# Kernel optimization log

Measured on AMD Instinct MI355X. Metric: run time of the kernel, lower is better.

## Reference

```python
import jax, jax.numpy as jnp
import numpy as np
import math

LS1 = [0, 1, 2]
LS2 = [0, 1, 2]
B = 1048576


def _fact(n):
    return math.factorial(n)


def _w3j_complex(j1, j2, j3, m1, m2, m3):
    # Racah formula for the complex-basis Wigner 3j symbol.
    if m1 + m2 + m3 != 0:
        return 0.0
    if not (abs(j1 - j2) <= j3 <= j1 + j2):
        return 0.0
    if abs(m1) > j1 or abs(m2) > j2 or abs(m3) > j3:
        return 0.0
    tmin = max(0, j2 - j3 - m1, j1 - j3 + m2)
    tmax = min(j1 + j2 - j3, j1 - m1, j2 + m2)
    s = 0.0
    for t in range(tmin, tmax + 1):
        s += (-1) ** t / (
            _fact(t) * _fact(j3 - j2 + t + m1) * _fact(j3 - j1 + t - m2)
            * _fact(j1 + j2 - j3 - t) * _fact(j1 - t - m1) * _fact(j2 - t + m2)
        )
    delta = math.sqrt(
        _fact(j1 + j2 - j3) * _fact(j1 - j2 + j3) * _fact(-j1 + j2 + j3)
        / _fact(j1 + j2 + j3 + 1)
    )
    pref = math.sqrt(
        _fact(j1 + m1) * _fact(j1 - m1) * _fact(j2 + m2) * _fact(j2 - m2)
        * _fact(j3 + m3) * _fact(j3 - m3)
    )
    return ((-1) ** (j1 - j2 - m3)) * delta * pref * s


def _U(l):
    # Unitary change of basis: complex spherical harmonics -> real spherical harmonics.
    d = 2 * l + 1
    U = np.zeros((d, d), dtype=complex)
    s = 1.0 / math.sqrt(2.0)
    for m in range(-l, l + 1):
        i = m + l
        if m > 0:
            U[i, m + l] = ((-1) ** m) * s
            U[i, -m + l] = s
        elif m == 0:
            U[i, l] = 1.0
        else:
            a = -m
            U[i, m + l] = 1j * s
            U[i, a + l] = -1j * ((-1) ** a) * s
    return U


def _real_w3j(l1, l2, l3):
    # Wigner 3j tensor in the real spherical-harmonic basis, Frobenius norm 1.
    W = np.zeros((2 * l1 + 1, 2 * l2 + 1, 2 * l3 + 1), dtype=complex)
    for m1 in range(-l1, l1 + 1):
        for m2 in range(-l2, l2 + 1):
            for m3 in range(-l3, l3 + 1):
                W[m1 + l1, m2 + l2, m3 + l3] = _w3j_complex(l1, l2, l3, m1, m2, m3)
    T = np.einsum('am,bn,co,mno->abc', _U(l1), _U(l2), _U(l3), W)
    re, im = T.real, T.imag
    T = re if np.abs(re).sum() >= np.abs(im).sum() else im
    return T.astype(np.float32)


def build_cb_matrix(ls1, ls2):
    # Faithful replication of EinsumTensorProduct.__init__ layout logic.
    layout = {}
    cb_height = 0
    idx1 = 0
    for l1 in ls1:
        idx2 = 0
        for l2 in ls2:
            for l3 in range(abs(l1 - l2), l1 + l2 + 1):
                layout.setdefault(l3, []).append((l1, l2, idx1, idx2))
                cb_height += 2 * l3 + 1
            idx2 += 2 * l2 + 1
        idx1 += 2 * l1 + 1
    dim1 = sum(2 * l + 1 for l in ls1)
    dim2 = sum(2 * l + 1 for l in ls2)
    cb = np.zeros((cb_height, dim1, dim2), dtype=np.float32)
    lmax2 = max(ls2)
    row = 0
    for l3 in sorted(layout.keys()):
        mults = sorted(layout[l3], key=lambda x: x[0] * lmax2 + x[1])
        for l1, l2, o1, o2 in mults:
            blk = _real_w3j(l1, l2, l3) * math.sqrt(2 * l3 + 1)  # [m1, m2, m3]
            cb[row:row + 2 * l3 + 1, o1:o1 + 2 * l1 + 1, o2:o2 + 2 * l2 + 1] = \
                np.transpose(blk, (2, 0, 1))
            row += 2 * l3 + 1
    return cb


def setup_inputs() -> dict:
    key = jax.random.key(0)
    k1, k2 = jax.random.split(key)
    dim1 = sum(2 * l + 1 for l in LS1)
    dim2 = sum(2 * l + 1 for l in LS2)
    cb = jnp.asarray(build_cb_matrix(LS1, LS2))  # [81, 9, 9]
    in1 = jax.random.normal(k1, (B, dim1), dtype=jnp.float32)
    in2 = jax.random.normal(k2, (B, dim2), dtype=jnp.float32)
    return {"in1": in1, "in2": in2, "cb_matrix": cb}


def reference(in1, in2, cb_matrix):
    # out[b, k] = sum_{i,j} in1[b, i] * in2[b, j] * cb[k, i, j]
    return jnp.einsum('bi,bj,kij->bk', in1, in2, cb_matrix)
```

## Files before the change

### kernel.cpp

```cpp
#include <hip/hip_runtime.h>
#include <stdint.h>

#define THREADS 192
#define ROWS_PER_ITER 192
#define DIM 9
#define NK 81
#define F 81
#define NCHUNK 6
#define NGROUP 12

typedef __attribute__((ext_vector_type(8))) short short8;
typedef __attribute__((ext_vector_type(16))) float f32x16;

__device__ inline unsigned short f32_bf16(float x) {
    unsigned u = __float_as_uint(x);
    u += 0x7FFFu + ((u >> 16) & 1u);
    return (unsigned short)(u >> 16);
}
__device__ inline float bf16_f32(unsigned short h) {
    return __uint_as_float(((unsigned)h) << 16);
}

__global__ __launch_bounds__(THREADS, 3)
void tp_mfma(const float* __restrict__ in1, const float* __restrict__ in2,
             const float* __restrict__ cb, float* __restrict__ out,
             int nrows, int niter) {
    __shared__ __attribute__((aligned(16))) unsigned short s_p[NGROUP * ROWS_PER_ITER * 8];

    const int tid  = threadIdx.x;
    const int lane = tid & 63;
    const int wave = tid >> 6;
    const int l31  = lane & 31;
    const int h    = lane >> 5;
    const int kcol = 32 * wave + l31;

    short8 Bhi[NCHUNK], Blo[NCHUNK];
    for (int c = 0; c < NCHUNK; ++c) {
        union { short8 v; unsigned short u[8]; } bh, bl;
        for (int j = 0; j < 8; ++j) {
            int f = c * 16 + h * 8 + j;
            float v = 0.0f;
            if (f < F && kcol < NK) v = cb[kcol * F + f];
            unsigned short hi = f32_bf16(v);
            bh.u[j] = (unsigned short)hi;
            bl.u[j] = f32_bf16(v - bf16_f32(hi));
        }
        Bhi[c] = bh.v; Blo[c] = bl.v;
    }

    for (int iter = blockIdx.x; iter < niter; iter += gridDim.x) {
        const long rowbase = (long)iter * ROWS_PER_ITER;
        const long row = rowbase + tid;

        __syncthreads();

        float a[DIM], b[DIM];
        if (row < nrows) {
            const float* p1 = in1 + row * DIM;
            const float* p2 = in2 + row * DIM;
#pragma unroll
            for (int i = 0; i < DIM; ++i) { a[i] = p1[i]; b[i] = p2[i]; }
        } else {
#pragma unroll
            for (int i = 0; i < DIM; ++i) { a[i] = 0.0f; b[i] = 0.0f; }
        }
#pragma unroll
        for (int g = 0; g < NGROUP; ++g) {
            unsigned int d[4];
#pragma unroll
            for (int q = 0; q < 4; ++q) {
                const int f0 = g * 8 + 2 * q, f1 = f0 + 1;
                unsigned short h0 = (f0 < F) ? f32_bf16(a[f0 / DIM] * b[f0 % DIM]) : (unsigned short)0;
                unsigned short h1 = (f1 < F) ? f32_bf16(a[f1 / DIM] * b[f1 % DIM]) : (unsigned short)0;
                d[q] = (unsigned)h0 | ((unsigned)h1 << 16);
            }
            ((uint4*)s_p)[g * ROWS_PER_ITER + tid] = make_uint4(d[0], d[1], d[2], d[3]);
        }
        __syncthreads();

#pragma unroll
        for (int st = 0; st < 6; ++st) {
            const int m0 = st * 32;
            f32x16 acc = {0.f,0.f,0.f,0.f, 0.f,0.f,0.f,0.f, 0.f,0.f,0.f,0.f, 0.f,0.f,0.f,0.f};
#pragma unroll
            for (int c = 0; c < NCHUNK; ++c) {
                const int cidx = c * 2 + h;
                short8 A = ((const short8*)s_p)[cidx * ROWS_PER_ITER + m0 + l31];
                acc = __builtin_amdgcn_mfma_f32_32x32x16_bf16(A, Bhi[c], acc, 0, 0, 0);
                acc = __builtin_amdgcn_mfma_f32_32x32x16_bf16(A, Blo[c], acc, 0, 0, 0);
            }
            if (kcol < NK) {
#pragma unroll
                for (int r = 0; r < 16; ++r) {
                    const int mrow = m0 + (r & 3) + 8 * (r >> 2) + 4 * h;
                    const long grow = rowbase + mrow;
                    if (grow < nrows) out[grow * NK + kcol] = acc[r];
                }
            }
        }
    }
}

extern "C" void kernel_launch(void* const* d_in, const int* in_sizes, int n_in,
                              void* d_out, int out_size, void* d_ws, size_t ws_size,
                              hipStream_t stream) {
    const float* in1 = (const float*)d_in[0];
    const float* in2 = (const float*)d_in[1];
    const float* cb  = (const float*)d_in[2];
    float* out = (float*)d_out;

    int nrows = in_sizes[0] / DIM;
    int niter = (nrows + ROWS_PER_ITER - 1) / ROWS_PER_ITER;

    tp_mfma<<<1024, THREADS, 0, stream>>>(in1, in2, cb, out, nrows, niter);
}
```

Baseline: 481.1 us.

## Double-buffer per-wave input tiles via async global-to-LDS loads, drop block barriers

Each block now handles 32-row tiles instead of 192-row batches. Every wave asynchronously stages the tile's in1/in2 rows into its own LDS double buffer with global_load_lds, prefetching the next tile while computing the current one. The bf16 outer-product A fragments are built in registers rather than round-tripping through shared memory, which removes both __syncthreads per iteration. Occupancy rises to 4 blocks per SIMD and the grid grows. In exchange, the three waves load the same input tile redundantly, relying on L2 to absorb the duplicate traffic, and the manual vmcnt wait must stay correct.

```diff
diff --git a/kernel.cpp b/kernel.cpp
--- a/kernel.cpp
+++ b/kernel.cpp
@@ -2,12 +2,12 @@
 #include <stdint.h>
 
 #define THREADS 192
-#define ROWS_PER_ITER 192
 #define DIM 9
 #define NK 81
 #define F 81
 #define NCHUNK 6
-#define NGROUP 12
+#define TILE 32
+#define GRID 1280
 
 typedef __attribute__((ext_vector_type(8))) short short8;
 typedef __attribute__((ext_vector_type(16))) float f32x16;
@@ -21,11 +21,11 @@
     return __uint_as_float(((unsigned)h) << 16);
 }
 
-__global__ __launch_bounds__(THREADS, 3)
+__global__ __launch_bounds__(THREADS, 4)
 void tp_mfma(const float* __restrict__ in1, const float* __restrict__ in2,
              const float* __restrict__ cb, float* __restrict__ out,
-             int nrows, int niter) {
-    __shared__ __attribute__((aligned(16))) unsigned short s_p[NGROUP * ROWS_PER_ITER * 8];
+             int nrows, int ntiles) {
+    __shared__ __attribute__((aligned(16))) float s_in[3][2][576];
 
     const int tid  = threadIdx.x;
     const int lane = tid & 63;
@@ -41,63 +41,104 @@
             int f = c * 16 + h * 8 + j;
             float v = 0.0f;
             if (f < F && kcol < NK) v = cb[kcol * F + f];
-            unsigned short hi = f32_bf16(v);
-            bh.u[j] = (unsigned short)hi;
-            bl.u[j] = f32_bf16(v - bf16_f32(hi));
+            unsigned short hb = f32_bf16(v);
+            bh.u[j] = hb;
+            bl.u[j] = f32_bf16(v - bf16_f32(hb));
         }
         Bhi[c] = bh.v; Blo[c] = bl.v;
     }
 
-    for (int iter = blockIdx.x; iter < niter; iter += gridDim.x) {
-        const long rowbase = (long)iter * ROWS_PER_ITER;
-        const long row = rowbase + tid;
+    const unsigned lim16 = (unsigned)nrows * 36u - 16u;
+    const unsigned lim4  = (unsigned)nrows * 36u - 4u;
+    const uintptr_t p1 = (uintptr_t)in1;
+    const uintptr_t p2 = (uintptr_t)in2;
 
-        __syncthreads();
+    auto stage = [&](int t, int buf) {
+        const unsigned tb = (unsigned)t * 1152u;
+        float* dst0 = &s_in[wave][buf][0];
+        {
+            unsigned o = tb + (unsigned)lane * 16u;
+            if (o > lim16) o = lim16;
+            __builtin_amdgcn_global_load_lds(
+                (__attribute__((address_space(1))) void*)(p1 + o),
+                (__attribute__((address_space(3))) void*)dst0, 16, 0, 0);
+        }
+        {
+            unsigned bb = 1024u + (unsigned)lane * 16u;
+            unsigned o1 = tb + bb;          if (o1 > lim16) o1 = lim16;
+            unsigned o2 = tb + bb - 1152u;  if (o2 > lim16) o2 = lim16;
+            uintptr_t src = (bb < 1152u) ? (p1 + o1) : (p2 + o2);
+            __builtin_amdgcn_global_load_lds(
+                (__attribute__((address_space(1))) void*)src,
+                (__attribute__((address_space(3))) void*)(dst0 + 256), 16, 0, 0);
+        }
+        {
+            unsigned o = tb + 896u + (unsigned)lane * 4u;
+            if (o > lim4) o = lim4;
+            __builtin_amdgcn_global_load_lds(
+                (__attribute__((address_space(1))) void*)(p2 + o),
+                (__attribute__((address_space(3))) void*)(dst0 + 512), 4, 0, 0);
+        }
+    };
 
+    int cur = 0;
+    const int t0 = blockIdx.x;
+    if (t0 < ntiles) stage(t0, 0);
+
+    for (int t = t0; t < ntiles; t += gridDim.x) {
+        const int tn = t + gridDim.x;
+        if (tn < ntiles) stage(tn, cur ^ 1);
+        asm volatile("s_waitcnt vmcnt(3)" ::: "memory");
+        __builtin_amdgcn_sched_barrier(0);
+
+        const float* sa = &s_in[wave][cur][0];
         float a[DIM], b[DIM];
-        if (row < nrows) {
-            const float* p1 = in1 + row * DIM;
-            const float* p2 = in2 + row * DIM;
 #pragma unroll
-            for (int i = 0; i < DIM; ++i) { a[i] = p1[i]; b[i] = p2[i]; }
-        } else {
+        for (int i = 0; i < DIM; ++i) {
+            a[i] = sa[l31 * 9 + i];
+            b[i] = sa[288 + l31 * 9 + i];
+        }
+
+        short8 A[NCHUNK];
 #pragma unroll
-            for (int i = 0; i < DIM; ++i) { a[i] = 0.0f; b[i] = 0.0f; }
+        for (int c = 0; c < NCHUNK; ++c) {
+            union { short8 v; unsigned short u[8]; } av;
+#pragma unroll
+            for (int j = 0; j < 8; ++j) {
+                const int f0 = c * 16 + j;
+                const int f1 = f0 + 8;
+                float q0 = (f0 < F) ? a[f0 / 9] * b[f0 % 9] : 0.0f;
+                float q1 = (f1 < F) ? a[f1 / 9] * b[f1 % 9] : 0.0f;
+                av.u[j] = f32_bf16(h ? q1 : q0);
+            }
+            A[c] = av.v;
         }
+
+        f32x16 acc = {0.f,0.f,0.f,0.f, 0.f,0.f,0.f,0.f, 0.f,0.f,0.f,0.f, 0.f,0.f,0.f,0.f};
 #pragma unroll
-        for (int g = 0; g < NGROUP; ++g) {
-            unsigned int d[4];
-#pragma unroll
-            for (int q = 0; q < 4; ++q) {
-                const int f0 = g * 8 + 2 * q, f1 = f0 + 1;
-                unsigned short h0 = (f0 < F) ? f32_bf16(a[f0 / DIM] * b[f0 % DIM]) : (unsigned short)0;
-                unsigned short h1 = (f1 < F) ? f32_bf16(a[f1 / DIM] * b[f1 % DIM]) : (unsigned short)0;
-                d[q] = (unsigned)h0 | ((unsigned)h1 << 16);
-            }
-            ((uint4*)s_p)[g * ROWS_PER_ITER + tid] = make_uint4(d[0], d[1], d[2], d[3]);
+        for (int c = 0; c < NCHUNK; ++c) {
+            acc = __builtin_amdgcn_mfma_f32_32x32x16_bf16(A[c], Bhi[c], acc, 0, 0, 0);
+            acc = __builtin_amdgcn_mfma_f32_32x32x16_bf16(A[c], Blo[c], acc, 0, 0, 0);
         }
-        __syncthreads();
 
-#pragma unroll
-        for (int st = 0; st < 6; ++st) {
-            const int m0 = st * 32;
-            f32x16 acc = {0.f,0.f,0.f,0.f, 0.f,0.f,0.f,0.f, 0.f,0.f,0.f,0.f, 0.f,0.f,0.f,0.f};
-#pragma unroll
-            for (int c = 0; c < NCHUNK; ++c) {
-                const int cidx = c * 2 + h;
-                short8 A = ((const short8*)s_p)[cidx * ROWS_PER_ITER + m0 + l31];
-                acc = __builtin_amdgcn_mfma_f32_32x32x16_bf16(A, Bhi[c], acc, 0, 0, 0);
-                acc = __builtin_amdgcn_mfma_f32_32x32x16_bf16(A, Blo[c], acc, 0, 0, 0);
-            }
-            if (kcol < NK) {
+        if (kcol < NK) {
+            const long r0 = (long)t * TILE;
+            float* po = out + r0 * NK + (h * 4) * NK + kcol;
+            if (r0 + TILE <= (long)nrows) {
 #pragma unroll
                 for (int r = 0; r < 16; ++r) {
-                    const int mrow = m0 + (r & 3) + 8 * (r >> 2) + 4 * h;
-                    const long grow = rowbase + mrow;
-                    if (grow < nrows) out[grow * NK + kcol] = acc[r];
+                    const int mrow = (r & 3) + 8 * (r >> 2);
+                    po[mrow * NK] = acc[r];
+                }
+            } else {
+#pragma unroll
+                for (int r = 0; r < 16; ++r) {
+                    const int mrow = (r & 3) + 8 * (r >> 2);
+                    if (r0 + mrow + 4 * h < (long)nrows) po[mrow * NK] = acc[r];
                 }
             }
         }
+        cur ^= 1;
     }
 }
 
@@ -109,8 +150,9 @@
     const float* cb  = (const float*)d_in[2];
     float* out = (float*)d_out;
 
-    int nrows = in_sizes[0] / DIM;
-    int niter = (nrows + ROWS_PER_ITER - 1) / ROWS_PER_ITER;
+    int nrows  = in_sizes[0] / DIM;
+    int ntiles = (nrows + TILE - 1) / TILE;
+    int grid = (GRID < ntiles) ? GRID : ntiles;
 
-    tp_mfma<<<1024, THREADS, 0, stream>>>(in1, in2, cb, out, nrows, niter);
+    tp_mfma<<<grid, THREADS, 0, stream>>>(in1, in2, cb, out, nrows, ntiles);
 }
```

New measurement: 508.3 us. 1.06x slower.
